# Kernel tuning notes

Hardware: AMD Instinct MI355X
Metric: run time of the kernel (lower is better)

## Reference

```python
import jax, jax.numpy as jnp
import numpy as np

D_MODEL = 1024
N_HEADS = 16
DEPTH = D_MODEL // N_HEADS
NEG_INF = -1.0e9


def setup_inputs() -> dict:
    key = jax.random.key(0)
    ks = jax.random.split(key, 11)
    B, S = 2, 2048
    xk = jax.random.normal(ks[0], (B, S, D_MODEL), jnp.float32)
    xq = jax.random.normal(ks[1], (B, S, D_MODEL), jnp.float32)
    xv = jax.random.normal(ks[2], (B, S, D_MODEL), jnp.float32)
    sc = 1.0 / np.sqrt(D_MODEL)
    wq = jax.random.normal(ks[3], (D_MODEL, D_MODEL), jnp.float32) * sc
    wk = jax.random.normal(ks[4], (D_MODEL, D_MODEL), jnp.float32) * sc
    wv = jax.random.normal(ks[5], (D_MODEL, D_MODEL), jnp.float32) * sc
    wo = jax.random.normal(ks[6], (D_MODEL, D_MODEL), jnp.float32) * sc
    bq = jnp.zeros((D_MODEL,), jnp.float32)
    bk = jnp.zeros((D_MODEL,), jnp.float32)
    bv = jnp.zeros((D_MODEL,), jnp.float32)
    bo = jnp.zeros((D_MODEL,), jnp.float32)
    return {"xk": xk, "xq": xq, "xv": xv, "wq": wq, "bq": bq, "wk": wk,
            "bk": bk, "wv": wv, "bv": bv, "wo": wo, "bo": bo}


def _split_heads(t):
    # [B, S, D] -> [B, H, S, depth]
    B, S, _ = t.shape
    return t.reshape(B, S, N_HEADS, DEPTH).transpose(0, 2, 1, 3)


def reference(xk, xq, xv, wq, bq, wk, bk, wv, bv, wo, bo):
    B, Sq, _ = xq.shape
    Sk = xk.shape[1]
    q = _split_heads(xq @ wq + bq)  # [B,H,Sq,d]
    k = _split_heads(xk @ wk + bk)  # [B,H,Sk,d]
    v = _split_heads(xv @ wv + bv)  # [B,H,Sk,d]
    logits = jnp.einsum('bhqd,bhkd->bhqk', q, k) / jnp.sqrt(
        jnp.asarray(DEPTH, q.dtype))
    # additive causal mask: (1 - lower_triangular) * -1e9
    causal = (1.0 - jnp.tril(jnp.ones((Sq, Sk), logits.dtype))) * NEG_INF
    logits = logits + causal[None, None, :, :]
    attn = jax.nn.softmax(logits, axis=-1)
    out = jnp.einsum('bhqk,bhkd->bhqd', attn, v)
    out = out.transpose(0, 2, 1, 3).reshape(B, Sq, D_MODEL)
    return out @ wo + bo
```

## Files before the change

### kernel.cpp

```cpp
#include <hip/hip_runtime.h>

typedef unsigned short u16;
typedef unsigned int u32;
typedef u16 u16x8 __attribute__((ext_vector_type(8)));
typedef u32 u32x2 __attribute__((ext_vector_type(2)));
typedef __bf16 bf16x8 __attribute__((ext_vector_type(8)));
typedef float f32x4 __attribute__((ext_vector_type(4)));

#define DM 1024
#define SEQ 2048
#define BATCH 2
#define MROWS 4096

__device__ __forceinline__ u16 f2bf(float f) {
  unsigned int x = __builtin_bit_cast(unsigned int, f);
  x += 0x7fffu + ((x >> 16) & 1u);
  return (u16)(x >> 16);
}
__device__ __forceinline__ u32 f2bf2(float lo, float hi) {
  return (u32)f2bf(lo) | ((u32)f2bf(hi) << 16);
}
__device__ __forceinline__ u32 pack2bf(float lo, float hi) {
  return __builtin_amdgcn_perm(__builtin_bit_cast(u32, hi),
                               __builtin_bit_cast(u32, lo), 0x07060302u);
}

__device__ __forceinline__ void gld16(const void* g, void* l) {
  __builtin_amdgcn_global_load_lds(
      (const __attribute__((address_space(1))) void*)g,
      (__attribute__((address_space(3))) void*)l, 16, 0, 0);
}

struct TrArgs { const float* in[4]; u16* out[4]; };

__global__ __launch_bounds__(256) void transpose_w4(TrArgs a) {
  const float* __restrict__ in = a.in[blockIdx.z];
  u16* __restrict__ out = a.out[blockIdx.z];
  __shared__ u16 T[64][72];
  int r0 = blockIdx.y * 64, c0 = blockIdx.x * 64;
  int t = threadIdx.x;
  int r = t >> 3, cg = (t & 7) * 8;
#pragma unroll
  for (int p = 0; p < 2; p++) {
    const float* src = in + (size_t)(r0 + r + p * 32) * DM + c0 + cg;
    f32x4 x0 = *(const f32x4*)src;
    f32x4 x1 = *(const f32x4*)(src + 4);
    u16x8 v;
#pragma unroll
    for (int j = 0; j < 4; j++) { v[j] = f2bf(x0[j]); v[4 + j] = f2bf(x1[j]); }
    *(u16x8*)(&T[r + p * 32][cg]) = v;
  }
  __syncthreads();
#pragma unroll
  for (int p = 0; p < 2; p++) {
    int orow = r + p * 32;
    u16x8 v;
#pragma unroll
    for (int j = 0; j < 8; j++) v[j] = T[cg + j][orow];
    *(u16x8*)(out + (size_t)(c0 + orow) * DM + r0 + cg) = v;
  }
}

struct GemmArgs { const void* A[3]; const u16* WT[3]; const float* bias[3]; void* C[3]; };

template <int MT, int NT, bool AF32, bool OF32, bool VT>
__global__ __launch_bounds__(256) void gemmT(GemmArgs g) {
  __shared__ __align__(16) u16 As[2][MT * 32 * 32];
  __shared__ __align__(16) u16 Bs[2][NT * 32 * 32];
  const int z = blockIdx.z;
  const u16* __restrict__ WT = g.WT[z];
  const int tid = threadIdx.x, lane = tid & 63, wave = tid >> 6;
  const int fr = lane & 15, kq = lane >> 4;
  const int mq = (wave >> 1) * (MT * 16), nq = (wave & 1) * (NT * 16);
  const int m0 = blockIdx.y * (MT * 32), n0 = blockIdx.x * (NT * 32);
  const int fo = ((kq ^ ((fr >> 1) & 3)) * 8);
  constexpr int AI = MT / 2, BI = NT / 2;
  f32x4 acc[MT][NT] = {};

  auto stage = [&](int buf, int kk) {
    if constexpr (AF32) {
      const float* A = (const float*)g.A[z];
#pragma unroll
      for (int i = 0; i < AI; i++) {
        int ci = i * 256 + tid, row = ci >> 2, sl = ci & 3;
        int sc = (sl ^ ((row >> 1) & 3)) * 8;
        const float* s0 = A + (size_t)(m0 + row) * DM + kk + sc;
        f32x4 a0 = *(const f32x4*)s0, a1 = *(const f32x4*)(s0 + 4);
        u16x8 v;
#pragma unroll
        for (int j = 0; j < 4; j++) { v[j] = f2bf(a0[j]); v[4 + j] = f2bf(a1[j]); }
        *(u16x8*)(As[buf] + ci * 8) = v;
      }
    } else {
      const u16* A = (const u16*)g.A[z];
#pragma unroll
      for (int i = 0; i < AI; i++) {
        int ci = i * 256 + tid, row = ci >> 2, sl = ci & 3;
        int sc = (sl ^ ((row >> 1) & 3)) * 8;
        gld16(A + (size_t)(m0 + row) * DM + kk + sc, As[buf] + ci * 8);
      }
    }
#pragma unroll
    for (int i = 0; i < BI; i++) {
      int ci = i * 256 + tid, row = ci >> 2, sl = ci & 3;
      int sc = (sl ^ ((row >> 1) & 3)) * 8;
      gld16(WT + (size_t)(n0 + row) * DM + kk + sc, Bs[buf] + ci * 8);
    }
  };

  stage(0, 0);
  __syncthreads();
  for (int k = 0; k < DM / 32; k++) {
    if (k + 1 < DM / 32) stage((k + 1) & 1, (k + 1) * 32);
    const int buf = k & 1;
    bf16x8 af[MT], bfr[NT];
#pragma unroll
    for (int mt = 0; mt < MT; mt++)
      af[mt] = __builtin_bit_cast(
          bf16x8, *(const u16x8*)(As[buf] + (mq + mt * 16 + fr) * 32 + fo));
#pragma unroll
    for (int nt = 0; nt < NT; nt++)
      bfr[nt] = __builtin_bit_cast(
          bf16x8, *(const u16x8*)(Bs[buf] + (nq + nt * 16 + fr) * 32 + fo));
#pragma unroll
    for (int mt = 0; mt < MT; mt++)
#pragma unroll
      for (int nt = 0; nt < NT; nt++)
        acc[mt][nt] = __builtin_amdgcn_mfma_f32_16x16x32_bf16(
            af[mt], bfr[nt], acc[mt][nt], 0, 0, 0);
    __syncthreads();
  }

  const float* __restrict__ bias = g.bias[z];
  const bool vtr = VT && (z == 2);
#pragma unroll
  for (int nt = 0; nt < NT; nt++) {
    int col = n0 + nq + nt * 16 + fr;
    float bb = bias[col];
#pragma unroll
    for (int mt = 0; mt < MT; mt++) {
      int row0 = m0 + mq + mt * 16 + kq * 4;
      if (vtr) {
        u32x2 d;
        d[0] = f2bf2(acc[mt][nt][0] + bb, acc[mt][nt][1] + bb);
        d[1] = f2bf2(acc[mt][nt][2] + bb, acc[mt][nt][3] + bb);
        size_t idx = ((size_t)((row0 >> 11) * 16 + (col >> 6)) * 64 +
                      (col & 63)) * SEQ + (row0 & 2047);
        *(u32x2*)((u16*)g.C[z] + idx) = d;
      } else {
#pragma unroll
        for (int r = 0; r < 4; r++) {
          float val = acc[mt][nt][r] + bb;
          if constexpr (OF32)
            ((float*)g.C[z])[(size_t)(row0 + r) * DM + col] = val;
          else
            ((u16*)g.C[z])[(size_t)(row0 + r) * DM + col] = f2bf(val);
        }
      }
    }
  }
}

__global__ __launch_bounds__(128) void attn5(u16* __restrict__ Q,
                                             const u16* __restrict__ K,
                                             const u16* __restrict__ Vtg) {
  __shared__ __align__(16) u16 Ksh[2][64 * 64];
  __shared__ __align__(16) u16 Vsh[2][64 * 64];
  __shared__ __align__(16) u16 Psh[64 * 64];
  __shared__ float Lbuf[2][32];
  const int tid = threadIdx.x, wq = tid >> 6, lane = tid & 63;
  const int fr = lane & 15, kq = lane >> 4, f7 = fr & 7;
  const int bh = blockIdx.x, b = bh >> 4, h = bh & 15;
  const int qt = 31 - blockIdx.y;
  const float C1 = 0.125f * 1.44269504f;

  int xo[2];
  xo[0] = (kq ^ f7) * 8;
  xo[1] = ((4 + kq) ^ f7) * 8;

  const u16* kp[4];
  const u16* vp[4];
#pragma unroll
  for (int i = 0; i < 4; i++) {
    int ci = i * 128 + tid, row = ci >> 3, sl = ci & 7;
    int sc = (sl ^ (row & 7)) * 8;
    kp[i] = K + (size_t)(b * SEQ + row) * DM + h * 64 + sc;
    vp[i] = Vtg + (size_t)(bh * 64 + row) * SEQ + sc;
  }
  auto stage = [&](int buf, int t) {
#pragma unroll
    for (int i = 0; i < 4; i++) {
      int ci = i * 128 + tid;
      gld16(kp[i] + (size_t)t * 64 * DM, Ksh[buf] + ci * 8);
      gld16(vp[i] + t * 64, Vsh[buf] + ci * 8);
    }
  };

  bf16x8 qf[2][2];
#pragma unroll
  for (int qtl = 0; qtl < 2; qtl++) {
    size_t qr = (size_t)(b * SEQ + qt * 64 + wq * 32 + qtl * 16 + fr) * DM + h * 64;
#pragma unroll
    for (int kk = 0; kk < 2; kk++)
      qf[qtl][kk] =
          __builtin_bit_cast(bf16x8, *(const u16x8*)(Q + qr + kk * 32 + kq * 8));
  }

  f32x4 ov[2][4] = {};
  float lac[2] = {0.f, 0.f};

  stage(0, 0);
  __syncthreads();
  for (int t = 0; t <= qt; t++) {
    if (t < qt) stage((t + 1) & 1, t + 1);
    const int buf = t & 1;

    f32x4 st[2][4];
#pragma unroll
    for (int kt = 0; kt < 4; kt++) {
      bf16x8 k0 = __builtin_bit_cast(
          bf16x8, *(const u16x8*)(Ksh[buf] + (kt * 16 + fr) * 64 + xo[0]));
      bf16x8 k1 = __builtin_bit_cast(
          bf16x8, *(const u16x8*)(Ksh[buf] + (kt * 16 + fr) * 64 + xo[1]));
#pragma unroll
      for (int qtl = 0; qtl < 2; qtl++) {
        f32x4 s = {};
        s = __builtin_amdgcn_mfma_f32_16x16x32_bf16(k0, qf[qtl][0], s, 0, 0, 0);
        s = __builtin_amdgcn_mfma_f32_16x16x32_bf16(k1, qf[qtl][1], s, 0, 0, 0);
        st[qtl][kt] = s;
      }
    }
    if (t == qt) {
#pragma unroll
      for (int qtl = 0; qtl < 2; qtl++)
#pragma unroll
        for (int kt = 0; kt < 4; kt++)
#pragma unroll
          for (int r = 0; r < 4; r++)
            if (kt * 16 + kq * 4 + r > wq * 32 + qtl * 16 + fr)
              st[qtl][kt][r] = -1e30f;
    }
#pragma unroll
    for (int qtl = 0; qtl < 2; qtl++) {
      float ls = 0.f;
      int prow = (wq * 32 + qtl * 16 + fr) * 64;
#pragma unroll
      for (int kt = 0; kt < 4; kt++) {
        float p0 = __builtin_amdgcn_exp2f(st[qtl][kt][0] * C1);
        float p1 = __builtin_amdgcn_exp2f(st[qtl][kt][1] * C1);
        float p2 = __builtin_amdgcn_exp2f(st[qtl][kt][2] * C1);
        float p3 = __builtin_amdgcn_exp2f(st[qtl][kt][3] * C1);
        ls += (p0 + p1) + (p2 + p3);
        u32x2 d;
        d[0] = pack2bf(p0, p1);
        d[1] = pack2bf(p2, p3);
        int sl = (2 * kt + (kq >> 1)) ^ f7;
        *(u32x2*)(Psh + prow + sl * 8 + (kq & 1) * 4) = d;
      }
      ls += __shfl_xor(ls, 16);
      ls += __shfl_xor(ls, 32);
      lac[qtl] += ls;
    }
#pragma unroll
    for (int kk = 0; kk < 2; kk++) {
      bf16x8 pa[2];
#pragma unroll
      for (int qtl = 0; qtl < 2; qtl++)
        pa[qtl] = __builtin_bit_cast(
            bf16x8,
            *(const u16x8*)(Psh + (wq * 32 + qtl * 16 + fr) * 64 + xo[kk]));
#pragma unroll
      for (int nt = 0; nt < 4; nt++) {
        bf16x8 vb = __builtin_bit_cast(
            bf16x8, *(const u16x8*)(Vsh[buf] + (nt * 16 + fr) * 64 + xo[kk]));
#pragma unroll
        for (int qtl = 0; qtl < 2; qtl++)
          ov[qtl][nt] = __builtin_amdgcn_mfma_f32_16x16x32_bf16(
              pa[qtl], vb, ov[qtl][nt], 0, 0, 0);
      }
    }
    __syncthreads();
  }
  if (kq == 0) {
    Lbuf[wq][fr] = lac[0];
    Lbuf[wq][16 + fr] = lac[1];
  }
#pragma unroll
  for (int qtl = 0; qtl < 2; qtl++) {
    float rinv[4];
#pragma unroll
    for (int r = 0; r < 4; r++)
      rinv[r] = 1.0f / Lbuf[wq][qtl * 16 + kq * 4 + r];
#pragma unroll
    for (int nt = 0; nt < 4; nt++)
#pragma unroll
      for (int r = 0; r < 4; r++) {
        int row = qt * 64 + wq * 32 + qtl * 16 + kq * 4 + r;
        Q[(size_t)(b * SEQ + row) * DM + h * 64 + nt * 16 + fr] =
            f2bf(ov[qtl][nt][r] * rinv[r]);
      }
  }
}

extern "C" void kernel_launch(void* const* d_in, const int* in_sizes, int n_in,
                              void* d_out, int out_size, void* d_ws,
                              size_t ws_size, hipStream_t stream) {
  const float* xk = (const float*)d_in[0];
  const float* xq = (const float*)d_in[1];
  const float* xv = (const float*)d_in[2];
  const float* wq = (const float*)d_in[3];
  const float* bq = (const float*)d_in[4];
  const float* wk = (const float*)d_in[5];
  const float* bk = (const float*)d_in[6];
  const float* wv = (const float*)d_in[7];
  const float* bv = (const float*)d_in[8];
  const float* wo = (const float*)d_in[9];
  const float* bo = (const float*)d_in[10];

  u16* Qb = (u16*)d_ws;
  u16* Kb = Qb + (size_t)MROWS * DM;
  u16* Vb = Kb + (size_t)MROWS * DM;
  u16* WTq = Vb + (size_t)MROWS * DM;
  u16* WTk = WTq + (size_t)DM * DM;
  u16* WTv = WTk + (size_t)DM * DM;
  u16* WTo = WTv + (size_t)DM * DM;

  dim3 blk(256);

  TrArgs tr;
  tr.in[0] = wq; tr.in[1] = wk; tr.in[2] = wv; tr.in[3] = wo;
  tr.out[0] = WTq; tr.out[1] = WTk; tr.out[2] = WTv; tr.out[3] = WTo;
  transpose_w4<<<dim3(16, 16, 4), blk, 0, stream>>>(tr);

  GemmArgs gq;
  gq.A[0] = xq; gq.A[1] = xk; gq.A[2] = xv;
  gq.WT[0] = WTq; gq.WT[1] = WTk; gq.WT[2] = WTv;
  gq.bias[0] = bq; gq.bias[1] = bk; gq.bias[2] = bv;
  gq.C[0] = Qb; gq.C[1] = Kb; gq.C[2] = Vb;
  gemmT<4, 4, true, false, true>
      <<<dim3(DM / 128, MROWS / 128, 3), blk, 0, stream>>>(gq);

  attn5<<<dim3(BATCH * 16, 32), dim3(128), 0, stream>>>(Qb, Kb, Vb);

  GemmArgs go;
  go.A[0] = Qb; go.WT[0] = WTo; go.bias[0] = bo; go.C[0] = d_out;
  go.A[1] = Qb; go.WT[1] = WTo; go.bias[1] = bo; go.C[1] = d_out;
  go.A[2] = Qb; go.WT[2] = WTo; go.bias[2] = bo; go.C[2] = d_out;
  gemmT<2, 4, false, true, false>
      <<<dim3(DM / 128, MROWS / 64, 1), blk, 0, stream>>>(go);
}
```

Measured before the change: 237.5 us.

## Pre-cast Q/K inputs, split V projection, add separate V transpose kernel

```diff
diff --git a/kernel.cpp b/kernel.cpp
--- a/kernel.cpp
+++ b/kernel.cpp
@@ -16,9 +16,6 @@
   unsigned int x = __builtin_bit_cast(unsigned int, f);
   x += 0x7fffu + ((x >> 16) & 1u);
   return (u16)(x >> 16);
-}
-__device__ __forceinline__ u32 f2bf2(float lo, float hi) {
-  return (u32)f2bf(lo) | ((u32)f2bf(hi) << 16);
 }
 __device__ __forceinline__ u32 pack2bf(float lo, float hi) {
   return __builtin_amdgcn_perm(__builtin_bit_cast(u32, hi),
@@ -61,23 +58,65 @@
   }
 }
 
+struct CastArgs { const float* in[2]; u16* out[2]; };
+
+__global__ __launch_bounds__(256) void cast_x(CastArgs a) {
+  const float* __restrict__ in = a.in[blockIdx.y];
+  u16* __restrict__ out = a.out[blockIdx.y];
+  size_t e = ((size_t)blockIdx.x * 256 + threadIdx.x) * 8;
+  f32x4 a0 = *(const f32x4*)(in + e);
+  f32x4 a1 = *(const f32x4*)(in + e + 4);
+  u16x8 v;
+#pragma unroll
+  for (int j = 0; j < 4; j++) { v[j] = f2bf(a0[j]); v[4 + j] = f2bf(a1[j]); }
+  *(u16x8*)(out + e) = v;
+}
+
+__global__ __launch_bounds__(256) void vtrans(const u16* __restrict__ V,
+                                              u16* __restrict__ Vt) {
+  __shared__ u16 T[64][72];
+  const int bh = blockIdx.y, b = bh >> 4, h = bh & 15;
+  const int s0 = blockIdx.x * 64;
+  const int t = threadIdx.x;
+  const int r = t >> 2, cg = (t & 3) * 16;
+  {
+    const u16* src = V + (size_t)(b * SEQ + s0 + r) * DM + h * 64 + cg;
+    *(u16x8*)(&T[r][cg]) = *(const u16x8*)src;
+    *(u16x8*)(&T[r][cg + 8]) = *(const u16x8*)(src + 8);
+  }
+  __syncthreads();
+  {
+    int d = r;
+    u16x8 v0, v1;
+#pragma unroll
+    for (int j = 0; j < 8; j++) {
+      v0[j] = T[cg + j][d];
+      v1[j] = T[cg + 8 + j][d];
+    }
+    u16* dst = Vt + (size_t)(bh * 64 + d) * SEQ + s0 + cg;
+    *(u16x8*)dst = v0;
+    *(u16x8*)(dst + 8) = v1;
+  }
+}
+
 struct GemmArgs { const void* A[3]; const u16* WT[3]; const float* bias[3]; void* C[3]; };
 
-template <int MT, int NT, bool AF32, bool OF32, bool VT>
+template <int MT, int NT, bool AF32, bool OF32>
 __global__ __launch_bounds__(256) void gemmT(GemmArgs g) {
-  __shared__ __align__(16) u16 As[2][MT * 32 * 32];
-  __shared__ __align__(16) u16 Bs[2][NT * 32 * 32];
+  __shared__ __align__(16) u16 As[MT * 32 * 32];
+  __shared__ __align__(16) u16 Bs[NT * 32 * 32];
   const int z = blockIdx.z;
   const u16* __restrict__ WT = g.WT[z];
   const int tid = threadIdx.x, lane = tid & 63, wave = tid >> 6;
   const int fr = lane & 15, kq = lane >> 4;
   const int mq = (wave >> 1) * (MT * 16), nq = (wave & 1) * (NT * 16);
-  const int m0 = blockIdx.y * (MT * 32), n0 = blockIdx.x * (NT * 32);
+  const int m0 = blockIdx.x * (MT * 32), n0 = blockIdx.y * (NT * 32);
   const int fo = ((kq ^ ((fr >> 1) & 3)) * 8);
   constexpr int AI = MT / 2, BI = NT / 2;
   f32x4 acc[MT][NT] = {};
 
-  auto stage = [&](int buf, int kk) {
+  for (int kk = 0; kk < DM; kk += 32) {
+    __syncthreads();
     if constexpr (AF32) {
       const float* A = (const float*)g.A[z];
 #pragma unroll
@@ -89,7 +128,7 @@
         u16x8 v;
 #pragma unroll
         for (int j = 0; j < 4; j++) { v[j] = f2bf(a0[j]); v[4 + j] = f2bf(a1[j]); }
-        *(u16x8*)(As[buf] + ci * 8) = v;
+        *(u16x8*)(As + ci * 8) = v;
       }
     } else {
       const u16* A = (const u16*)g.A[z];
@@ -97,67 +136,49 @@
       for (int i = 0; i < AI; i++) {
         int ci = i * 256 + tid, row = ci >> 2, sl = ci & 3;
         int sc = (sl ^ ((row >> 1) & 3)) * 8;
-        gld16(A + (size_t)(m0 + row) * DM + kk + sc, As[buf] + ci * 8);
+        gld16(A + (size_t)(m0 + row) * DM + kk + sc, As + ci * 8);
       }
     }
 #pragma unroll
     for (int i = 0; i < BI; i++) {
       int ci = i * 256 + tid, row = ci >> 2, sl = ci & 3;
       int sc = (sl ^ ((row >> 1) & 3)) * 8;
-      gld16(WT + (size_t)(n0 + row) * DM + kk + sc, Bs[buf] + ci * 8);
-    }
-  };
-
-  stage(0, 0);
-  __syncthreads();
-  for (int k = 0; k < DM / 32; k++) {
-    if (k + 1 < DM / 32) stage((k + 1) & 1, (k + 1) * 32);
-    const int buf = k & 1;
+      gld16(WT + (size_t)(n0 + row) * DM + kk + sc, Bs + ci * 8);
+    }
+    __syncthreads();
     bf16x8 af[MT], bfr[NT];
 #pragma unroll
     for (int mt = 0; mt < MT; mt++)
       af[mt] = __builtin_bit_cast(
-          bf16x8, *(const u16x8*)(As[buf] + (mq + mt * 16 + fr) * 32 + fo));
+          bf16x8, *(const u16x8*)(As + (mq + mt * 16 + fr) * 32 + fo));
 #pragma unroll
     for (int nt = 0; nt < NT; nt++)
       bfr[nt] = __builtin_bit_cast(
-          bf16x8, *(const u16x8*)(Bs[buf] + (nq + nt * 16 + fr) * 32 + fo));
+          bf16x8, *(const u16x8*)(Bs + (nq + nt * 16 + fr) * 32 + fo));
 #pragma unroll
     for (int mt = 0; mt < MT; mt++)
 #pragma unroll
       for (int nt = 0; nt < NT; nt++)
         acc[mt][nt] = __builtin_amdgcn_mfma_f32_16x16x32_bf16(
             af[mt], bfr[nt], acc[mt][nt], 0, 0, 0);
-    __syncthreads();
   }
 
   const float* __restrict__ bias = g.bias[z];
-  const bool vtr = VT && (z == 2);
 #pragma unroll
   for (int nt = 0; nt < NT; nt++) {
     int col = n0 + nq + nt * 16 + fr;
     float bb = bias[col];
 #pragma unroll
-    for (int mt = 0; mt < MT; mt++) {
-      int row0 = m0 + mq + mt * 16 + kq * 4;
-      if (vtr) {
-        u32x2 d;
-        d[0] = f2bf2(acc[mt][nt][0] + bb, acc[mt][nt][1] + bb);
-        d[1] = f2bf2(acc[mt][nt][2] + bb, acc[mt][nt][3] + bb);
-        size_t idx = ((size_t)((row0 >> 11) * 16 + (col >> 6)) * 64 +
-                      (col & 63)) * SEQ + (row0 & 2047);
-        *(u32x2*)((u16*)g.C[z] + idx) = d;
-      } else {
-#pragma unroll
-        for (int r = 0; r < 4; r++) {
-          float val = acc[mt][nt][r] + bb;
-          if constexpr (OF32)
-            ((float*)g.C[z])[(size_t)(row0 + r) * DM + col] = val;
-          else
-            ((u16*)g.C[z])[(size_t)(row0 + r) * DM + col] = f2bf(val);
-        }
-      }
-    }
+    for (int mt = 0; mt < MT; mt++)
+#pragma unroll
+      for (int r = 0; r < 4; r++) {
+        int row = m0 + mq + mt * 16 + kq * 4 + r;
+        float val = acc[mt][nt][r] + bb;
+        if constexpr (OF32)
+          ((float*)g.C[z])[(size_t)row * DM + col] = val;
+        else
+          ((u16*)g.C[z])[(size_t)row * DM + col] = f2bf(val);
+      }
   }
 }
 
@@ -324,6 +345,9 @@
   u16* WTk = WTq + (size_t)DM * DM;
   u16* WTv = WTk + (size_t)DM * DM;
   u16* WTo = WTv + (size_t)DM * DM;
+  u16* Xq = (u16*)d_out;
+  u16* Xk = Xq + (size_t)MROWS * DM;
+  u16* Vtg = (u16*)d_out;
 
   dim3 blk(256);
 
@@ -332,20 +356,35 @@
   tr.out[0] = WTq; tr.out[1] = WTk; tr.out[2] = WTv; tr.out[3] = WTo;
   transpose_w4<<<dim3(16, 16, 4), blk, 0, stream>>>(tr);
 
-  GemmArgs gq;
-  gq.A[0] = xq; gq.A[1] = xk; gq.A[2] = xv;
-  gq.WT[0] = WTq; gq.WT[1] = WTk; gq.WT[2] = WTv;
-  gq.bias[0] = bq; gq.bias[1] = bk; gq.bias[2] = bv;
-  gq.C[0] = Qb; gq.C[1] = Kb; gq.C[2] = Vb;
-  gemmT<4, 4, true, false, true>
-      <<<dim3(DM / 128, MROWS / 128, 3), blk, 0, stream>>>(gq);
-
-  attn5<<<dim3(BATCH * 16, 32), dim3(128), 0, stream>>>(Qb, Kb, Vb);
+  CastArgs ca;
+  ca.in[0] = xq; ca.in[1] = xk;
+  ca.out[0] = Xq; ca.out[1] = Xk;
+  cast_x<<<dim3(MROWS * DM / 2048, 2), blk, 0, stream>>>(ca);
+
+  GemmArgs gqk;
+  gqk.A[0] = Xq; gqk.A[1] = Xk;
+  gqk.WT[0] = WTq; gqk.WT[1] = WTk;
+  gqk.bias[0] = bq; gqk.bias[1] = bk;
+  gqk.C[0] = Qb; gqk.C[1] = Kb;
+  gqk.A[2] = Xq; gqk.WT[2] = WTq; gqk.bias[2] = bq; gqk.C[2] = Qb;
+  gemmT<4, 4, false, false>
+      <<<dim3(MROWS / 128, DM / 128, 2), blk, 0, stream>>>(gqk);
+
+  GemmArgs gv;
+  gv.A[0] = xv; gv.WT[0] = WTv; gv.bias[0] = bv; gv.C[0] = Vb;
+  gv.A[1] = xv; gv.WT[1] = WTv; gv.bias[1] = bv; gv.C[1] = Vb;
+  gv.A[2] = xv; gv.WT[2] = WTv; gv.bias[2] = bv; gv.C[2] = Vb;
+  gemmT<4, 4, true, false>
+      <<<dim3(MROWS / 128, DM / 128, 1), blk, 0, stream>>>(gv);
+
+  vtrans<<<dim3(SEQ / 64, BATCH * 16), blk, 0, stream>>>(Vb, Vtg);
+
+  attn5<<<dim3(BATCH * 16, 32), dim3(128), 0, stream>>>(Qb, Kb, Vtg);
 
   GemmArgs go;
   go.A[0] = Qb; go.WT[0] = WTo; go.bias[0] = bo; go.C[0] = d_out;
   go.A[1] = Qb; go.WT[1] = WTo; go.bias[1] = bo; go.C[1] = d_out;
   go.A[2] = Qb; go.WT[2] = WTo; go.bias[2] = bo; go.C[2] = d_out;
-  gemmT<2, 4, false, true, false>
-      <<<dim3(DM / 128, MROWS / 64, 1), blk, 0, stream>>>(go);
-}
+  gemmT<2, 4, false, true>
+      <<<dim3(MROWS / 64, DM / 128, 1), blk, 0, stream>>>(go);
+}
```

New measurement: 251.4 us. 5.8% more time.
